# Performance work log

Hardware: AMD Instinct MI355X
Metric: run time of the kernel (lower is better)

## Reference

```python
import jax, jax.numpy as jnp
import numpy as np

ALPHA = 0.2  # leaky_relu negative slope (init arg `alpha`)
V_NODES = 7

def setup_inputs() -> dict:
    key = jax.random.key(0)
    k1, k2, k3 = jax.random.split(key, 3)
    N, C, T, V = 256, 256, 64, V_NODES
    IN, OUT = C * T, 256
    h = jax.random.normal(k1, (N, C, T, V), dtype=jnp.float32)
    # xavier_uniform with gain=1.414
    limW = 1.414 * np.sqrt(6.0 / (IN + OUT))
    W = jax.random.uniform(k2, (IN, OUT), dtype=jnp.float32, minval=-limW, maxval=limW)
    lima = 1.414 * np.sqrt(6.0 / (2 * OUT + 1))
    a = jax.random.uniform(k3, (2 * OUT, 1), dtype=jnp.float32, minval=-lima, maxval=lima)
    Bp = jnp.zeros((V, V), dtype=jnp.float32)  # torch: zeros(7,7)+1e-6; the 1e-6 is added in reference
    return {"h": h, "W": W, "a": a, "Bp": Bp}

def reference(h, W, a, Bp):
    N, C, T, V = h.shape
    E = W.shape[1]
    # (N,C,T,V) -> (N,V,C*T)
    hf = jnp.transpose(h, (0, 3, 1, 2)).reshape(N, V, C * T)
    Wh = jnp.einsum('nvi,io->nvo', hf, W)  # [N,V,E]
    # pairwise concat score [Wh_i || Wh_j] @ a  ==  Wh_i@a1 + Wh_j@a2 (exact same math, no O(V^2*2E) tensor)
    a1, a2 = a[:E, 0], a[E:, 0]
    s1 = Wh @ a1  # [N,V] (score contribution of row node i)
    s2 = Wh @ a2  # [N,V] (score contribution of col node j)
    e = jax.nn.leaky_relu(s1[:, :, None] + s2[:, None, :], negative_slope=ALPHA)  # [N,V,V]
    attention = jax.nn.softmax(e, axis=-1)
    # learned adjacency: B + I, min-max normalized, sym-normalized D^-1/2 A D^-1/2
    adj = (Bp + 1e-6) + jnp.eye(V, dtype=Bp.dtype)
    adj = (adj - adj.min()) / (adj.max() - adj.min())
    D = jnp.diag(jnp.sum(adj, axis=1))
    D12 = jnp.sqrt(jnp.linalg.inv(D))  # diag -> elementwise sqrt of 1/deg on diagonal
    adj_norm = D12 @ adj @ D12  # [V,V]
    attention = jnp.einsum('ij,njk->nik', adj_norm, attention)  # [N,V,V]
    h_prime = jnp.einsum('nij,njo->nio', attention, Wh)  # [N,V,E]
    return jax.nn.elu(h_prime)
```

## Files before the change

### kernel.cpp

```cpp
#include <hip/hip_runtime.h>
#include <cstdint>

#define CC 256
#define TT 64
#define VV 7
#define KK 16384
#define EE 256
#define LRELU_ALPHA 0.2f

typedef __bf16 bf16x8 __attribute__((ext_vector_type(8)));
typedef float f32x4 __attribute__((ext_vector_type(4)));

#define PARTIAL_OFF 0u
#define WT_OFF (8u*256u*2048u*4u)
#define ADJ_OFF (WT_OFF + 256u*16384u*2u)

__device__ __forceinline__ unsigned short f2bf(float f){
  union { float f; unsigned u; } x; x.f = f;
  unsigned r = x.u + 0x7fffu + ((x.u >> 16) & 1u);
  return (unsigned short)(r >> 16);
}

__global__ __launch_bounds__(256) void k_transpose_w(const float* __restrict__ W,
                                                     unsigned short* __restrict__ Wt){
  __shared__ float tile[64][65];
  const int i0 = blockIdx.x * 64;
  const int o0 = blockIdx.y * 64;
  const int tid = threadIdx.x;
  #pragma unroll
  for (int r = 0; r < 16; ++r){
    int il = r*4 + (tid >> 6);
    int ol = tid & 63;
    tile[il][ol] = W[(size_t)(i0+il)*EE + o0 + ol];
  }
  __syncthreads();
  #pragma unroll
  for (int r = 0; r < 16; ++r){
    int ol = r*4 + (tid >> 6);
    int il = tid & 63;
    Wt[(size_t)(o0+ol)*KK + i0 + il] = f2bf(tile[il][ol]);
  }
}

__global__ void k_adj(const float* __restrict__ Bp, float* __restrict__ adjn){
  if (threadIdx.x == 0 && blockIdx.x == 0){
    float adj[49];
    float mn = 1e30f, mx = -1e30f;
    for (int i = 0; i < 7; ++i)
      for (int j = 0; j < 7; ++j){
        float x = Bp[i*7+j] + 1e-6f + (i == j ? 1.f : 0.f);
        adj[i*7+j] = x;
        mn = fminf(mn, x); mx = fmaxf(mx, x);
      }
    float inv = 1.f / (mx - mn);
    for (int i = 0; i < 49; ++i) adj[i] = (adj[i] - mn) * inv;
    float d12[7];
    for (int i = 0; i < 7; ++i){
      float s = 0.f;
      for (int j = 0; j < 7; ++j) s += adj[i*7+j];
      d12[i] = 1.f / sqrtf(s);
    }
    for (int i = 0; i < 7; ++i)
      for (int j = 0; j < 7; ++j)
        adjn[i*7+j] = d12[i] * adj[i*7+j] * d12[j];
  }
}

__global__ __launch_bounds__(256) void k_gemm(const float* __restrict__ h,
                                              const unsigned short* __restrict__ Wt,
                                              float* __restrict__ part){
  __shared__ unsigned short As[256*72];
  __shared__ unsigned short Bs[64*72];
  const int tid  = threadIdx.x;
  const int mt   = blockIdx.x;
  const int kc   = blockIdx.y;
  const int n0   = mt * 8;
  const int w    = tid >> 6;
  const int lane = tid & 63;
  const int col  = lane & 15;
  const int quad = lane >> 4;

  for (int idx = tid; idx < 8*72; idx += 256) Bs[56*72 + idx] = 0;

  int hoff[14], hlds[14];
  #pragma unroll
  for (int it = 0; it < 14; ++it){
    int j  = tid + it*256;
    int nn = j / 448;
    int rr = j - nn*448;
    int t_ = rr / 7;
    int v_ = rr - t_*7;
    hoff[it] = (n0+nn)*114688 + rr;
    hlds[it] = (nn*7 + v_)*72 + t_;
  }
  const int wo = tid >> 3;
  const int wk = (tid & 7) * 8;

  f32x4 acc[4][4];
  #pragma unroll
  for (int a_ = 0; a_ < 4; ++a_)
    #pragma unroll
    for (int b_ = 0; b_ < 4; ++b_)
      acc[a_][b_] = (f32x4){0.f, 0.f, 0.f, 0.f};

  for (int s = 0; s < 32; ++s){
    const int c  = kc*32 + s;
    const int i0 = c*64;
    {
      const unsigned short* src = Wt + (size_t)wo*KK + i0 + wk;
      #pragma unroll
      for (int r = 0; r < 8; ++r){
        float4 v = *reinterpret_cast<const float4*>(src + (size_t)r*32*KK);
        *reinterpret_cast<float4*>(&As[(wo + r*32)*72 + wk]) = v;
      }
    }
    {
      const int cb = c*448;
      #pragma unroll
      for (int it = 0; it < 14; ++it){
        float val = h[(size_t)(hoff[it] + cb)];
        Bs[hlds[it]] = f2bf(val);
      }
    }
    __syncthreads();
    #pragma unroll
    for (int kh = 0; kh < 2; ++kh){
      bf16x8 af[4], bfr[4];
      #pragma unroll
      for (int oi = 0; oi < 4; ++oi)
        af[oi] = *reinterpret_cast<const bf16x8*>(&As[(w*64 + oi*16 + col)*72 + kh*32 + quad*8]);
      #pragma unroll
      for (int mi = 0; mi < 4; ++mi)
        bfr[mi] = *reinterpret_cast<const bf16x8*>(&Bs[(mi*16 + col)*72 + kh*32 + quad*8]);
      #pragma unroll
      for (int oi = 0; oi < 4; ++oi)
        #pragma unroll
        for (int mi = 0; mi < 4; ++mi)
          acc[oi][mi] = __builtin_amdgcn_mfma_f32_16x16x32_bf16(af[oi], bfr[mi], acc[oi][mi], 0, 0, 0);
    }
    __syncthreads();
  }

  #pragma unroll
  for (int oi = 0; oi < 4; ++oi){
    #pragma unroll
    for (int r = 0; r < 4; ++r){
      int o = w*64 + oi*16 + quad*4 + r;
      size_t rowbase = ((size_t)(kc*256 + o))*2048 + mt*64;
      #pragma unroll
      for (int mi = 0; mi < 4; ++mi)
        part[rowbase + mi*16 + col] = acc[oi][mi][r];
    }
  }
}

__global__ __launch_bounds__(256) void k_attn(const float* __restrict__ part,
                                              const float* __restrict__ a,
                                              const float* __restrict__ adjn,
                                              float* __restrict__ out){
  const int n    = blockIdx.x;
  const int tid  = threadIdx.x;
  const int lane = tid & 63;
  const int wv   = tid >> 6;
  const int mt   = n >> 3;
  const int nn   = n & 7;
  const int bm   = mt*64 + nn*7;

  float wh[7];
  #pragma unroll
  for (int v = 0; v < 7; ++v){
    float s = 0.f;
    #pragma unroll
    for (int k = 0; k < 8; ++k)
      s += part[((size_t)(k*256 + tid))*2048 + bm + v];
    wh[v] = s;
  }

  const float a1 = a[tid];
  const float a2 = a[256 + tid];

  __shared__ float red1[4][7], red2[4][7];
  __shared__ float s1s[7], s2s[7];
  __shared__ float att0[49], att[49];

  #pragma unroll
  for (int v = 0; v < 7; ++v){
    float x1 = wh[v]*a1;
    float x2 = wh[v]*a2;
    #pragma unroll
    for (int off = 32; off > 0; off >>= 1){
      x1 += __shfl_down(x1, off);
      x2 += __shfl_down(x2, off);
    }
    if (lane == 0){ red1[wv][v] = x1; red2[wv][v] = x2; }
  }
  __syncthreads();
  if (tid < 7){
    s1s[tid] = red1[0][tid]+red1[1][tid]+red1[2][tid]+red1[3][tid];
    s2s[tid] = red2[0][tid]+red2[1][tid]+red2[2][tid]+red2[3][tid];
  }
  __syncthreads();
  if (tid < 7){
    const int v = tid;
    float e[7]; float mx = -1e30f;
    #pragma unroll
    for (int u = 0; u < 7; ++u){
      float t = s1s[v] + s2s[u];
      t = t > 0.f ? t : LRELU_ALPHA*t;
      e[u] = t; mx = fmaxf(mx, t);
    }
    float sum = 0.f;
    #pragma unroll
    for (int u = 0; u < 7; ++u){ e[u] = expf(e[u]-mx); sum += e[u]; }
    float inv = 1.f/sum;
    #pragma unroll
    for (int u = 0; u < 7; ++u) att0[v*7+u] = e[u]*inv;
  }
  __syncthreads();
  if (tid < 7){
    const int v = tid;
    #pragma unroll
    for (int u = 0; u < 7; ++u){
      float s = 0.f;
      #pragma unroll
      for (int w7 = 0; w7 < 7; ++w7) s += adjn[v*7+w7]*att0[w7*7+u];
      att[v*7+u] = s;
    }
  }
  __syncthreads();
  #pragma unroll
  for (int v = 0; v < 7; ++v){
    float hp = 0.f;
    #pragma unroll
    for (int u = 0; u < 7; ++u) hp += att[v*7+u]*wh[u];
    float o = hp > 0.f ? hp : expm1f(hp);
    out[(size_t)(n*7+v)*256 + tid] = o;
  }
}

extern "C" void kernel_launch(void* const* d_in, const int* in_sizes, int n_in,
                              void* d_out, int out_size, void* d_ws, size_t ws_size,
                              hipStream_t stream){
  const float* h  = (const float*)d_in[0];
  const float* W  = (const float*)d_in[1];
  const float* a  = (const float*)d_in[2];
  const float* Bp = (const float*)d_in[3];
  float* out = (float*)d_out;
  char* ws = (char*)d_ws;
  float*          part = (float*)(ws + PARTIAL_OFF);
  unsigned short* Wt   = (unsigned short*)(ws + WT_OFF);
  float*          adjn = (float*)(ws + ADJ_OFF);

  k_transpose_w<<<dim3(256, 4), 256, 0, stream>>>(W, Wt);
  k_adj<<<1, 64, 0, stream>>>(Bp, adjn);
  k_gemm<<<dim3(32, 8), 256, 0, stream>>>(h, Wt, part);
  k_attn<<<256, 256, 0, stream>>>(part, a, adjn, out);
}
```

Measured before the change: 239.9 us.

## Widen GEMM split-K with atomic accumulation, vectorize h loads, fuse adjacency

The GEMM grid grows from 32x8 to 32x32 blocks, each covering a quarter of the previous K range. Partial results are now accumulated with atomicAdd into a single zeroed Wh buffer (zeroed inside the transpose kernel) rather than written as 8 partial slabs and summed later. h is read with float4 loads instead of scalar loads. The adjacency normalization is folded into the attention kernel, which drops one launch. This gives more parallelism across the device and less partial-buffer traffic, at the cost of atomic contention and nondeterministic summation order.

```diff
diff --git a/kernel.cpp b/kernel.cpp
--- a/kernel.cpp
+++ b/kernel.cpp
@@ -1,9 +1,6 @@
 #include <hip/hip_runtime.h>
 #include <cstdint>
 
-#define CC 256
-#define TT 64
-#define VV 7
 #define KK 16384
 #define EE 256
 #define LRELU_ALPHA 0.2f
@@ -11,9 +8,8 @@
 typedef __bf16 bf16x8 __attribute__((ext_vector_type(8)));
 typedef float f32x4 __attribute__((ext_vector_type(4)));
 
-#define PARTIAL_OFF 0u
-#define WT_OFF (8u*256u*2048u*4u)
-#define ADJ_OFF (WT_OFF + 256u*16384u*2u)
+#define WH_OFF 0u
+#define WT_OFF (256u*2048u*4u)
 
 __device__ __forceinline__ unsigned short f2bf(float f){
   union { float f; unsigned u; } x; x.f = f;
@@ -22,11 +18,16 @@
 }
 
 __global__ __launch_bounds__(256) void k_transpose_w(const float* __restrict__ W,
-                                                     unsigned short* __restrict__ Wt){
+                                                     unsigned short* __restrict__ Wt,
+                                                     float* __restrict__ Wh){
   __shared__ float tile[64][65];
   const int i0 = blockIdx.x * 64;
   const int o0 = blockIdx.y * 64;
   const int tid = threadIdx.x;
+
+  const int bid = blockIdx.y * gridDim.x + blockIdx.x;
+  reinterpret_cast<float2*>(Wh)[bid * 256 + tid] = make_float2(0.f, 0.f);
+
   #pragma unroll
   for (int r = 0; r < 16; ++r){
     int il = r*4 + (tid >> 6);
@@ -42,8 +43,121 @@
   }
 }
 
-__global__ void k_adj(const float* __restrict__ Bp, float* __restrict__ adjn){
-  if (threadIdx.x == 0 && blockIdx.x == 0){
+__global__ __launch_bounds__(256) void k_gemm(const float* __restrict__ h,
+                                              const unsigned short* __restrict__ Wt,
+                                              float* __restrict__ Wh){
+  __shared__ unsigned short As[256*72];
+  __shared__ unsigned short Bs[64*72];
+  const int tid  = threadIdx.x;
+  const int mt   = blockIdx.x;
+  const int kc   = blockIdx.y;
+  const int n0   = mt * 8;
+  const int w    = tid >> 6;
+  const int lane = tid & 63;
+  const int col  = lane & 15;
+  const int quad = lane >> 4;
+
+  for (int idx = tid; idx < 8*72; idx += 256) Bs[56*72 + idx] = 0;
+
+  int hoff[4]; int hlds[4][4]; bool hval[4];
+  #pragma unroll
+  for (int it = 0; it < 4; ++it){
+    int j = tid + it*256;
+    hval[it] = (j < 896);
+    int jj = hval[it] ? j : 0;
+    int nn = jj / 112;
+    int f  = jj - nn*112;
+    hoff[it] = (n0+nn)*114688 + f*4;
+    #pragma unroll
+    for (int e = 0; e < 4; ++e){
+      int rr = f*4 + e;
+      int t_ = rr / 7;
+      int v_ = rr - t_*7;
+      hlds[it][e] = (nn*7 + v_)*72 + t_;
+    }
+  }
+  const int wo = tid >> 3;
+  const int wk = (tid & 7) * 8;
+
+  f32x4 acc[4][4];
+  #pragma unroll
+  for (int a_ = 0; a_ < 4; ++a_)
+    #pragma unroll
+    for (int b_ = 0; b_ < 4; ++b_)
+      acc[a_][b_] = (f32x4){0.f, 0.f, 0.f, 0.f};
+
+  for (int s = 0; s < 8; ++s){
+    const int c  = kc*8 + s;
+    const int i0 = c*64;
+    {
+      const unsigned short* src = Wt + (size_t)wo*KK + i0 + wk;
+      #pragma unroll
+      for (int r = 0; r < 8; ++r){
+        float4 v = *reinterpret_cast<const float4*>(src + (size_t)r*32*KK);
+        *reinterpret_cast<float4*>(&As[(wo + r*32)*72 + wk]) = v;
+      }
+    }
+    {
+      const int cb = c*448;
+      #pragma unroll
+      for (int it = 0; it < 4; ++it){
+        if (hval[it]){
+          float4 v = *reinterpret_cast<const float4*>(h + (size_t)(hoff[it] + cb));
+          Bs[hlds[it][0]] = f2bf(v.x);
+          Bs[hlds[it][1]] = f2bf(v.y);
+          Bs[hlds[it][2]] = f2bf(v.z);
+          Bs[hlds[it][3]] = f2bf(v.w);
+        }
+      }
+    }
+    __syncthreads();
+    #pragma unroll
+    for (int kh = 0; kh < 2; ++kh){
+      bf16x8 af[4], bfr[4];
+      #pragma unroll
+      for (int oi = 0; oi < 4; ++oi)
+        af[oi] = *reinterpret_cast<const bf16x8*>(&As[(w*64 + oi*16 + col)*72 + kh*32 + quad*8]);
+      #pragma unroll
+      for (int mi = 0; mi < 4; ++mi)
+        bfr[mi] = *reinterpret_cast<const bf16x8*>(&Bs[(mi*16 + col)*72 + kh*32 + quad*8]);
+      #pragma unroll
+      for (int oi = 0; oi < 4; ++oi)
+        #pragma unroll
+        for (int mi = 0; mi < 4; ++mi)
+          acc[oi][mi] = __builtin_amdgcn_mfma_f32_16x16x32_bf16(af[oi], bfr[mi], acc[oi][mi], 0, 0, 0);
+    }
+    __syncthreads();
+  }
+
+  #pragma unroll
+  for (int oi = 0; oi < 4; ++oi){
+    #pragma unroll
+    for (int r = 0; r < 4; ++r){
+      int o = w*64 + oi*16 + quad*4 + r;
+      size_t rowbase = (size_t)o*2048 + mt*64;
+      #pragma unroll
+      for (int mi = 0; mi < 4; ++mi)
+        atomicAdd(&Wh[rowbase + mi*16 + col], acc[oi][mi][r]);
+    }
+  }
+}
+
+__global__ __launch_bounds__(256) void k_attn(const float* __restrict__ Wh,
+                                              const float* __restrict__ a,
+                                              const float* __restrict__ Bp,
+                                              float* __restrict__ out){
+  const int n    = blockIdx.x;
+  const int tid  = threadIdx.x;
+  const int lane = tid & 63;
+  const int wv   = tid >> 6;
+  const int bm   = (n >> 3)*64 + (n & 7)*7;
+
+  __shared__ float adjn[49];
+  __shared__ float red1[4][7], red2[4][7];
+  __shared__ float s1s[7], s2s[7];
+  __shared__ float att0[49], att[49];
+
+  if (tid == 0){
     float adj[49];
     float mn = 1e30f, mx = -1e30f;
     for (int i = 0; i < 7; ++i)
@@ -64,124 +178,14 @@
       for (int j = 0; j < 7; ++j)
         adjn[i*7+j] = d12[i] * adj[i*7+j] * d12[j];
   }
-}
-
-__global__ __launch_bounds__(256) void k_gemm(const float* __restrict__ h,
-                                              const unsigned short* __restrict__ Wt,
-                                              float* __restrict__ part){
-  __shared__ unsigned short As[256*72];
-  __shared__ unsigned short Bs[64*72];
-  const int tid  = threadIdx.x;
-  const int mt   = blockIdx.x;
-  const int kc   = blockIdx.y;
-  const int n0   = mt * 8;
-  const int w    = tid >> 6;
-  const int lane = tid & 63;
-  const int col  = lane & 15;
-  const int quad = lane >> 4;
-
-  for (int idx = tid; idx < 8*72; idx += 256) Bs[56*72 + idx] = 0;
-
-  int hoff[14], hlds[14];
-  #pragma unroll
-  for (int it = 0; it < 14; ++it){
-    int j  = tid + it*256;
-    int nn = j / 448;
-    int rr = j - nn*448;
-    int t_ = rr / 7;
-    int v_ = rr - t_*7;
-    hoff[it] = (n0+nn)*114688 + rr;
-    hlds[it] = (nn*7 + v_)*72 + t_;
-  }
-  const int wo = tid >> 3;
-  const int wk = (tid & 7) * 8;
-
-  f32x4 acc[4][4];
-  #pragma unroll
-  for (int a_ = 0; a_ < 4; ++a_)
-    #pragma unroll
-    for (int b_ = 0; b_ < 4; ++b_)
-      acc[a_][b_] = (f32x4){0.f, 0.f, 0.f, 0.f};
-
-  for (int s = 0; s < 32; ++s){
-    const int c  = kc*32 + s;
-    const int i0 = c*64;
-    {
-      const unsigned short* src = Wt + (size_t)wo*KK + i0 + wk;
-      #pragma unroll
-      for (int r = 0; r < 8; ++r){
-        float4 v = *reinterpret_cast<const float4*>(src + (size_t)r*32*KK);
-        *reinterpret_cast<float4*>(&As[(wo + r*32)*72 + wk]) = v;
-      }
-    }
-    {
-      const int cb = c*448;
-      #pragma unroll
-      for (int it = 0; it < 14; ++it){
-        float val = h[(size_t)(hoff[it] + cb)];
-        Bs[hlds[it]] = f2bf(val);
-      }
-    }
-    __syncthreads();
-    #pragma unroll
-    for (int kh = 0; kh < 2; ++kh){
-      bf16x8 af[4], bfr[4];
-      #pragma unroll
-      for (int oi = 0; oi < 4; ++oi)
-        af[oi] = *reinterpret_cast<const bf16x8*>(&As[(w*64 + oi*16 + col)*72 + kh*32 + quad*8]);
-      #pragma unroll
-      for (int mi = 0; mi < 4; ++mi)
-        bfr[mi] = *reinterpret_cast<const bf16x8*>(&Bs[(mi*16 + col)*72 + kh*32 + quad*8]);
-      #pragma unroll
-      for (int oi = 0; oi < 4; ++oi)
-        #pragma unroll
-        for (int mi = 0; mi < 4; ++mi)
-          acc[oi][mi] = __builtin_amdgcn_mfma_f32_16x16x32_bf16(af[oi], bfr[mi], acc[oi][mi], 0, 0, 0);
-    }
-    __syncthreads();
-  }
-
-  #pragma unroll
-  for (int oi = 0; oi < 4; ++oi){
-    #pragma unroll
-    for (int r = 0; r < 4; ++r){
-      int o = w*64 + oi*16 + quad*4 + r;
-      size_t rowbase = ((size_t)(kc*256 + o))*2048 + mt*64;
-      #pragma unroll
-      for (int mi = 0; mi < 4; ++mi)
-        part[rowbase + mi*16 + col] = acc[oi][mi][r];
-    }
-  }
-}
-
-__global__ __launch_bounds__(256) void k_attn(const float* __restrict__ part,
-                                              const float* __restrict__ a,
-                                              const float* __restrict__ adjn,
-                                              float* __restrict__ out){
-  const int n    = blockIdx.x;
-  const int tid  = threadIdx.x;
-  const int lane = tid & 63;
-  const int wv   = tid >> 6;
-  const int mt   = n >> 3;
-  const int nn   = n & 7;
-  const int bm   = mt*64 + nn*7;
 
   float wh[7];
   #pragma unroll
-  for (int v = 0; v < 7; ++v){
-    float s = 0.f;
-    #pragma unroll
-    for (int k = 0; k < 8; ++k)
-      s += part[((size_t)(k*256 + tid))*2048 + bm + v];
-    wh[v] = s;
-  }
+  for (int v = 0; v < 7; ++v)
+    wh[v] = Wh[(size_t)tid*2048 + bm + v];
 
   const float a1 = a[tid];
   const float a2 = a[256 + tid];
-
-  __shared__ float red1[4][7], red2[4][7];
-  __shared__ float s1s[7], s2s[7];
-  __shared__ float att0[49], att[49];
 
   #pragma unroll
   for (int v = 0; v < 7; ++v){
@@ -247,12 +251,10 @@
   const float* Bp = (const float*)d_in[3];
   float* out = (float*)d_out;
   char* ws = (char*)d_ws;
-  float*          part = (float*)(ws + PARTIAL_OFF);
-  unsigned short* Wt   = (unsigned short*)(ws + WT_OFF);
-  float*          adjn = (float*)(ws + ADJ_OFF);
-
-  k_transpose_w<<<dim3(256, 4), 256, 0, stream>>>(W, Wt);
-  k_adj<<<1, 64, 0, stream>>>(Bp, adjn);
-  k_gemm<<<dim3(32, 8), 256, 0, stream>>>(h, Wt, part);
-  k_attn<<<256, 256, 0, stream>>>(part, a, adjn, out);
-}
+  float*          Wh = (float*)(ws + WH_OFF);
+  unsigned short* Wt = (unsigned short*)(ws + WT_OFF);
+
+  k_transpose_w<<<dim3(256, 4), 256, 0, stream>>>(W, Wt, Wh);
+  k_gemm<<<dim3(32, 32), 256, 0, stream>>>(h, Wt, Wh);
+  k_attn<<<256, 256, 0, stream>>>(Wh, a, Bp, out);
+}
```

New measurement: 287.6 us. 1.2x slower.
